# Optimization experiments

Measured on AMD Instinct MI355X. Metric: run time of the kernel, lower is better.

Reference implementation:

```python
import jax, jax.numpy as jnp
import numpy as np

B, N, D = 32, 1024, 768
E_TOK, E_CH, TOP_K = 4, 4, 2
E = E_TOK + E_CH
HN, HD = 4 * N, 4 * D  # hidden dims of token / channel mixers


def setup_inputs() -> dict:
    key = jax.random.key(0)
    ks = jax.random.split(key, 10)
    s = 0.02
    return {
        "x": jax.random.normal(ks[0], (B, N, D), jnp.float32),
        "router_w": jax.random.normal(ks[1], (E, D), jnp.float32) * s,
        # token mixers: fc1 (N->HN), fc2 (HN->N), stacked over E_TOK experts
        "tok_w1": jax.random.normal(ks[2], (E_TOK, HN, N), jnp.float32) * s,
        "tok_b1": jnp.zeros((E_TOK, HN), jnp.float32),
        "tok_w2": jax.random.normal(ks[3], (E_TOK, N, HN), jnp.float32) * s,
        "tok_b2": jnp.zeros((E_TOK, N), jnp.float32),
        # channel mixers: fc1 (D->HD), fc2 (HD->D), stacked over E_CH experts
        "ch_w1": jax.random.normal(ks[4], (E_CH, HD, D), jnp.float32) * s,
        "ch_b1": jnp.zeros((E_CH, HD), jnp.float32),
        "ch_w2": jax.random.normal(ks[5], (E_CH, D, HD), jnp.float32) * s,
        "ch_b2": jnp.zeros((E_CH, D), jnp.float32),
    }


def _gelu(x):
    return jax.nn.gelu(x, approximate=True)  # matches nn.GELU(approximate='tanh')


def reference(x, router_w, tok_w1, tok_b1, tok_w2, tok_b2, ch_w1, ch_b1, ch_w2, ch_b2):
    b = x.shape[0]
    # --- router: mean-pooled tokens -> logits over 8 experts ---
    router_logits = x.mean(axis=1) @ router_w.T                 # (B, E)
    router_probs = jax.nn.softmax(router_logits, axis=-1)
    top_w, top_i = jax.lax.top_k(router_probs, TOP_K)           # (B, k)
    top_w = top_w / top_w.sum(axis=-1, keepdims=True)
    # per-sample dense combine weights: zero for unselected experts
    combine = jnp.zeros((b, E), x.dtype).at[
        jnp.arange(b)[:, None], top_i
    ].add(top_w)                                                # (B, E)

    # --- token mixer experts (mix across N), stacked over experts ---
    xt = x.transpose(0, 2, 1)                                    # (B, D, N)
    h = _gelu(jnp.einsum('bdn,ehn->ebdh', xt, tok_w1) + tok_b1[:, None, None, :])
    tok_out = (jnp.einsum('ebdh,enh->ebdn', h, tok_w2)
               + tok_b2[:, None, None, :]).transpose(0, 1, 3, 2)  # (E_tok, B, N, D)

    # --- channel mixer experts (mix across D) ---
    g = _gelu(jnp.einsum('bnd,ehd->ebnh', x, ch_w1) + ch_b1[:, None, None, :])
    ch_out = jnp.einsum('ebnh,edh->ebnd', g, ch_w2) + ch_b2[:, None, None, :]  # (E_ch, B, N, D)

    all_out = jnp.concatenate([tok_out, ch_out], axis=0)        # (E, B, N, D)
    output = jnp.einsum('ebnd,be->bnd', all_out, combine)

    # --- Switch-style load-balancing aux loss ---
    top1 = top_i[:, 0]
    expert_mask = jax.nn.one_hot(top1, E, dtype=x.dtype)        # (B, E)
    aux_loss = E * jnp.sum(router_probs.mean(axis=0) * expert_mask.mean(axis=0))
    return output, aux_loss
```

## Files before the change

### kernel.cpp

```cpp
#include <hip/hip_runtime.h>
#include <cstdint>
#include <cstddef>

#define Bsz 32
#define Nn 1024
#define Dd 768
#define NE_TOK 4
#define NE 8
#define HN 4096
#define HD 3072
#define INTER_ELEMS (768 * 4096)
#define CHUNK 16

typedef __bf16 bf16x8 __attribute__((ext_vector_type(8)));
typedef float f32x4 __attribute__((ext_vector_type(4)));
typedef unsigned int __attribute__((address_space(1))) as1_uint;
typedef unsigned int __attribute__((address_space(3))) as3_uint;

__device__ __forceinline__ unsigned short f2bf(float f) {
  union { float f; unsigned u; } c; c.f = f;
  unsigned u = c.u;
  u += 0x7fffu + ((u >> 16) & 1u);
  return (unsigned short)(u >> 16);
}

__device__ __forceinline__ float gelu_f(float x) {
  float t = tanhf(0.7978845608028654f * (x + 0.044715f * x * x * x));
  return 0.5f * x * (1.0f + t);
}

__device__ __forceinline__ void async_cp16(const unsigned short* g, unsigned short* l) {
  __builtin_amdgcn_global_load_lds((as1_uint*)(void*)g, (as3_uint*)(void*)l, 16, 0, 0);
}

__device__ __forceinline__ void gemm_core(const unsigned short* Ag, const unsigned short* Bg,
                                          int K, int tm, int tn,
                                          unsigned short* sA, unsigned short* sB,
                                          f32x4 acc[4][4]) {
  const int tid = threadIdx.x;
  const int wave = tid >> 6;
  const int lane = tid & 63;
  const int wr = (wave >> 1) * 64;
  const int wc = (wave & 1) * 64;

  f32x4 zero = {0.f, 0.f, 0.f, 0.f};
#pragma unroll
  for (int i = 0; i < 4; ++i)
#pragma unroll
    for (int j = 0; j < 4; ++j) acc[i][j] = zero;

  const int q0 = wave * 2, q1 = wave * 2 + 1;
  const int c0 = q0 * 64 + lane, c1 = q1 * 64 + lane;
  const int ar0 = c0 >> 2, as0 = (c0 & 3) * 8;
  const int ar1 = c1 >> 2, as1 = (c1 & 3) * 8;
  const unsigned short* Ag0 = Ag + (size_t)(tm * 128 + ar0) * K + as0;
  const unsigned short* Ag1 = Ag + (size_t)(tm * 128 + ar1) * K + as1;
  const unsigned short* Bg0 = Bg + (size_t)(tn * 128 + ar0) * K + as0;
  const unsigned short* Bg1 = Bg + (size_t)(tn * 128 + ar1) * K + as1;
  unsigned short* sA0 = sA + q0 * 512;
  unsigned short* sA1 = sA + q1 * 512;
  unsigned short* sB0 = sB + q0 * 512;
  unsigned short* sB1 = sB + q1 * 512;

  const int fro = (lane & 15) * 32 + (lane >> 4) * 8;

  for (int k0 = 0; k0 < K; k0 += 32) {
    async_cp16(Ag0 + k0, sA0);
    async_cp16(Ag1 + k0, sA1);
    async_cp16(Bg0 + k0, sB0);
    async_cp16(Bg1 + k0, sB1);
    __syncthreads();

    bf16x8 a[4], bb[4];
#pragma unroll
    for (int i = 0; i < 4; ++i)
      a[i] = *(const bf16x8*)(sA + (wr + i * 16) * 32 + fro);
#pragma unroll
    for (int j = 0; j < 4; ++j)
      bb[j] = *(const bf16x8*)(sB + (wc + j * 16) * 32 + fro);
#pragma unroll
    for (int i = 0; i < 4; ++i)
#pragma unroll
      for (int j = 0; j < 4; ++j)
        acc[i][j] = __builtin_amdgcn_mfma_f32_16x16x32_bf16(a[i], bb[j], acc[i][j], 0, 0, 0);
    __syncthreads();
  }
}


__global__ void mean_kernel(const float* __restrict__ x, float* __restrict__ xmean) {
  int idx = blockIdx.x * 256 + threadIdx.x;
  int b = idx / Dd, d = idx - b * Dd;
  const float* p = x + (size_t)b * Nn * Dd + d;
  float s = 0.f;
#pragma unroll 8
  for (int n = 0; n < Nn; ++n) s += p[(size_t)n * Dd];
  xmean[idx] = s * (1.0f / Nn);
}

__global__ void router_kernel(const float* __restrict__ xmean, const float* __restrict__ rw,
                              int* __restrict__ topi, float* __restrict__ topw,
                              float* __restrict__ aux_out) {
  __shared__ float probs[Bsz][NE];
  __shared__ int top1[Bsz];
  int t = threadIdx.x;
  for (int p = t; p < Bsz * NE; p += 64) {
    int b = p >> 3, e = p & 7;
    const float* xm = xmean + b * Dd;
    const float* w = rw + e * Dd;
    float s = 0.f;
    for (int i = 0; i < Dd; ++i) s += xm[i] * w[i];
    probs[b][e] = s;
  }
  __syncthreads();
  if (t < Bsz) {
    float mx = -1e30f;
    for (int e = 0; e < NE; ++e) mx = fmaxf(mx, probs[t][e]);
    float pe[NE]; float sum = 0.f;
    for (int e = 0; e < NE; ++e) { pe[e] = expf(probs[t][e] - mx); sum += pe[e]; }
    float inv = 1.f / sum;
    for (int e = 0; e < NE; ++e) { pe[e] *= inv; probs[t][e] = pe[e]; }
    int i0 = 0;
    for (int e = 1; e < NE; ++e) if (pe[e] > pe[i0]) i0 = e;
    int i1 = (i0 == 0) ? 1 : 0;
    for (int e = 0; e < NE; ++e) if (e != i0 && pe[e] > pe[i1]) i1 = e;
    float ws2 = pe[i0] + pe[i1];
    topi[t * 2] = i0; topi[t * 2 + 1] = i1;
    topw[t * 2] = pe[i0] / ws2; topw[t * 2 + 1] = pe[i1] / ws2;
    top1[t] = i0;
  }
  __syncthreads();
  if (t == 0) {
    float aux = 0.f;
    for (int e = 0; e < NE; ++e) {
      float pm = 0.f; int cnt = 0;
      for (int b = 0; b < Bsz; ++b) { pm += probs[b][e]; if (top1[b] == e) cnt++; }
      aux += (pm / Bsz) * ((float)cnt / Bsz);
    }
    aux_out[0] = aux * NE;
  }
}

__global__ void convert_kernel(const float* __restrict__ src, unsigned short* __restrict__ dst,
                               int n4) {
  int i = blockIdx.x * 256 + threadIdx.x;
  if (i < n4) {
    const float4 v = ((const float4*)src)[i];
    ushort4 o = make_ushort4(f2bf(v.x), f2bf(v.y), f2bf(v.z), f2bf(v.w));
    ((ushort4*)dst)[i] = o;
  }
}

__global__ void transpose_kernel(const float* __restrict__ x,
                                 unsigned short* __restrict__ xbf,
                                 unsigned short* __restrict__ xtbf) {
  __shared__ unsigned short tile[64][66];
  const int b = blockIdx.z;
  const int d0 = blockIdx.x * 64;
  const int n0 = blockIdx.y * 64;
  const int tc = threadIdx.x & 63;
  const int tr = threadIdx.x >> 6;
  const float* xb = x + (size_t)b * Nn * Dd;
#pragma unroll
  for (int i = 0; i < 16; ++i) {
    int row = tr * 16 + i;
    unsigned short v = f2bf(xb[(size_t)(n0 + row) * Dd + d0 + tc]);
    tile[row][tc] = v;
    xbf[(size_t)b * Nn * Dd + (size_t)(n0 + row) * Dd + d0 + tc] = v;
  }
  __syncthreads();
#pragma unroll
  for (int i = 0; i < 16; ++i) {
    int drow = tr * 16 + i;
    xtbf[(size_t)b * Dd * Nn + (size_t)(d0 + drow) * Nn + n0 + tc] = tile[tc][drow];
  }
}

__global__ __launch_bounds__(256, 2) void l1_kernel(
    const unsigned short* __restrict__ xbf, const unsigned short* __restrict__ xtbf,
    const unsigned short* __restrict__ w1t, const unsigned short* __restrict__ w1c,
    const float* __restrict__ b1t, const float* __restrict__ b1c,
    const int* __restrict__ topi, unsigned short* __restrict__ inter, int slot, int b0) {
  __shared__ unsigned short sA[4096];
  __shared__ unsigned short sB[4096];
  const int y = blockIdx.y;
  const int b = b0 + y;
  const int e = topi[b * 2 + slot];
  const int tile = blockIdx.x;
  const unsigned short *A, *Bm;
  const float* bias;
  int K, ldc, tm, tn;
  if (e < NE_TOK) {
    A = xtbf + (size_t)b * Dd * Nn;
    Bm = w1t + (size_t)e * HN * Nn;
    bias = b1t + e * HN;
    K = Nn; ldc = HN;
    tm = tile >> 5; tn = tile & 31;
  } else {
    A = xbf + (size_t)b * Nn * Dd;
    Bm = w1c + (size_t)(e - 4) * HD * Dd;
    bias = b1c + (e - 4) * HD;
    K = Dd; ldc = HD;
    tm = tile / 24; tn = tile - tm * 24;
  }
  unsigned short* C = inter + (size_t)y * INTER_ELEMS;
  f32x4 acc[4][4];
  gemm_core(A, Bm, K, tm, tn, sA, sB, acc);

  const int lane = threadIdx.x & 63, wave = threadIdx.x >> 6;
  const int wr = (wave >> 1) * 64, wc = (wave & 1) * 64;
  const int r0 = tm * 128 + wr + (lane >> 4) * 4;
  const int c0 = tn * 128 + wc + (lane & 15);
#pragma unroll
  for (int i = 0; i < 4; ++i)
#pragma unroll
    for (int j = 0; j < 4; ++j) {
      int col = c0 + j * 16;
      float bcol = bias[col];
#pragma unroll
      for (int r = 0; r < 4; ++r) {
        int row = r0 + i * 16 + r;
        float v = acc[i][j][r] + bcol;
        C[(size_t)row * ldc + col] = f2bf(gelu_f(v));
      }
    }
}

__global__ __launch_bounds__(256, 2) void l2_kernel(
    const unsigned short* __restrict__ inter,
    const unsigned short* __restrict__ w2t, const unsigned short* __restrict__ w2c,
    const float* __restrict__ b2t, const float* __restrict__ b2c,
    const int* __restrict__ topi, const float* __restrict__ topw,
    float* __restrict__ out, int slot, int b0) {
  __shared__ unsigned short sA[4096];
  __shared__ unsigned short sB[4096];
  const int y = blockIdx.y;
  const int b = b0 + y;
  const int e = topi[b * 2 + slot];
  const float wgt = topw[b * 2 + slot];
  const int tile = blockIdx.x;
  const int tm = tile / 6, tn = tile - tm * 6;
  const bool tok = (e < NE_TOK);
  const unsigned short* ib = inter + (size_t)y * INTER_ELEMS;
  const unsigned short *A, *Bm;
  int K;
  if (tok) { A = w2t + (size_t)e * Nn * HN; Bm = ib; K = HN; }
  else     { A = ib; Bm = w2c + (size_t)(e - 4) * Dd * HD; K = HD; }
  f32x4 acc[4][4];
  gemm_core(A, Bm, K, tm, tn, sA, sB, acc);

  float* C = out + (size_t)b * Nn * Dd;
  const int lane = threadIdx.x & 63, wave = threadIdx.x >> 6;
  const int wr = (wave >> 1) * 64, wc = (wave & 1) * 64;
  const int r0 = tm * 128 + wr + (lane >> 4) * 4;
  const int c0 = tn * 128 + wc + (lane & 15);
#pragma unroll
  for (int i = 0; i < 4; ++i)
#pragma unroll
    for (int j = 0; j < 4; ++j) {
      int col = c0 + j * 16;
#pragma unroll
      for (int r = 0; r < 4; ++r) {
        int row = r0 + i * 16 + r;
        float bias = tok ? b2t[e * Nn + row] : b2c[(e - 4) * Dd + col];
        float v = (acc[i][j][r] + bias) * wgt;
        size_t idx = (size_t)row * Dd + col;
        if (slot == 0) C[idx] = v;
        else           C[idx] += v;
      }
    }
}

extern "C" void kernel_launch(void* const* d_in, const int* in_sizes, int n_in,
                              void* d_out, int out_size, void* d_ws, size_t ws_size,
                              hipStream_t stream) {
  const float* x       = (const float*)d_in[0];
  const float* rw      = (const float*)d_in[1];
  const float* tok_w1  = (const float*)d_in[2];
  const float* tok_b1  = (const float*)d_in[3];
  const float* tok_w2  = (const float*)d_in[4];
  const float* tok_b2  = (const float*)d_in[5];
  const float* ch_w1   = (const float*)d_in[6];
  const float* ch_b1   = (const float*)d_in[7];
  const float* ch_w2   = (const float*)d_in[8];
  const float* ch_b2   = (const float*)d_in[9];
  float* out = (float*)d_out;

  char* ws = (char*)d_ws;
  float* xmean = (float*)ws;            ws += (size_t)Bsz * Dd * 4;
  int* topi    = (int*)ws;              ws += 256;
  float* topw  = (float*)ws;            ws += 256;
  unsigned short* xbf  = (unsigned short*)ws; ws += (size_t)Bsz * Nn * Dd * 2;
  unsigned short* xtbf = (unsigned short*)ws; ws += (size_t)Bsz * Nn * Dd * 2;
  unsigned short* w1t  = (unsigned short*)ws; ws += (size_t)NE_TOK * HN * Nn * 2;
  unsigned short* w2t  = (unsigned short*)ws; ws += (size_t)NE_TOK * Nn * HN * 2;
  unsigned short* w1c  = (unsigned short*)ws; ws += (size_t)NE_TOK * HD * Dd * 2;
  unsigned short* w2c  = (unsigned short*)ws; ws += (size_t)NE_TOK * Dd * HD * 2;
  unsigned short* inter = (unsigned short*)ws;

  mean_kernel<<<(Bsz * Dd) / 256, 256, 0, stream>>>(x, xmean);
  router_kernel<<<1, 64, 0, stream>>>(xmean, rw, topi, topw, out + (size_t)Bsz * Nn * Dd);
  convert_kernel<<<16384, 256, 0, stream>>>(tok_w1, w1t, (NE_TOK * HN * Nn) / 4);
  convert_kernel<<<16384, 256, 0, stream>>>(tok_w2, w2t, (NE_TOK * Nn * HN) / 4);
  convert_kernel<<<9216, 256, 0, stream>>>(ch_w1, w1c, (NE_TOK * HD * Dd) / 4);
  convert_kernel<<<9216, 256, 0, stream>>>(ch_w2, w2c, (NE_TOK * Dd * HD) / 4);
  transpose_kernel<<<dim3(12, 16, Bsz), 256, 0, stream>>>(x, xbf, xtbf);

  for (int slot = 0; slot < 2; ++slot)
    for (int c = 0; c < 2; ++c) {
      l1_kernel<<<dim3(192, CHUNK), 256, 0, stream>>>(xbf, xtbf, w1t, w1c, tok_b1, ch_b1,
                                                      topi, inter, slot, c * CHUNK);
      l2_kernel<<<dim3(48, CHUNK), 256, 0, stream>>>(inter, w2t, w2c, tok_b2, ch_b2,
                                                     topi, topw, out, slot, c * CHUNK);
    }
}
```

Measured before the change: 1.761 ms.

## Double-buffer GEMM shared tiles and XOR-swizzle LDS layout

The GEMM core now keeps two shared-memory buffers, so the async copy of the next K tile is issued before the MFMAs on the current tile, and there is one barrier per iteration instead of two. The position of each 16-byte chunk in LDS is XOR-swizzled on both the write side and the fragment-read side to cut bank conflicts. Shared memory per block doubles to 32 KB, which may limit occupancy. Correctness depends on the async copies having completed by the barrier.

```diff
diff --git a/kernel.cpp b/kernel.cpp
--- a/kernel.cpp
+++ b/kernel.cpp
@@ -51,8 +51,8 @@
 
   const int q0 = wave * 2, q1 = wave * 2 + 1;
   const int c0 = q0 * 64 + lane, c1 = q1 * 64 + lane;
-  const int ar0 = c0 >> 2, as0 = (c0 & 3) * 8;
-  const int ar1 = c1 >> 2, as1 = (c1 & 3) * 8;
+  const int ar0 = c0 >> 2, as0 = ((c0 ^ (c0 >> 3)) & 3) * 8;
+  const int ar1 = c1 >> 2, as1 = ((c1 ^ (c1 >> 3)) & 3) * 8;
   const unsigned short* Ag0 = Ag + (size_t)(tm * 128 + ar0) * K + as0;
   const unsigned short* Ag1 = Ag + (size_t)(tm * 128 + ar1) * K + as1;
   const unsigned short* Bg0 = Bg + (size_t)(tn * 128 + ar0) * K + as0;
@@ -62,28 +62,41 @@
   unsigned short* sB0 = sB + q0 * 512;
   unsigned short* sB1 = sB + q1 * 512;
 
-  const int fro = (lane & 15) * 32 + (lane >> 4) * 8;
-
+  const int swz = ((lane >> 4) ^ (lane >> 1)) & 3;
+  const int fro = (lane & 15) * 32 + swz * 8;
+
+  async_cp16(Ag0, sA0);
+  async_cp16(Ag1, sA1);
+  async_cp16(Bg0, sB0);
+  async_cp16(Bg1, sB1);
+  __syncthreads();
+
+  int cur = 0;
   for (int k0 = 0; k0 < K; k0 += 32) {
-    async_cp16(Ag0 + k0, sA0);
-    async_cp16(Ag1 + k0, sA1);
-    async_cp16(Bg0 + k0, sB0);
-    async_cp16(Bg1 + k0, sB1);
-    __syncthreads();
-
+    const int k1 = k0 + 32;
+    if (k1 < K) {
+      const int nb = (cur ^ 1) * 4096;
+      async_cp16(Ag0 + k1, sA0 + nb);
+      async_cp16(Ag1 + k1, sA1 + nb);
+      async_cp16(Bg0 + k1, sB0 + nb);
+      async_cp16(Bg1 + k1, sB1 + nb);
+    }
+    const unsigned short* pA = sA + cur * 4096;
+    const unsigned short* pB = sB + cur * 4096;
     bf16x8 a[4], bb[4];
 #pragma unroll
     for (int i = 0; i < 4; ++i)
-      a[i] = *(const bf16x8*)(sA + (wr + i * 16) * 32 + fro);
+      a[i] = *(const bf16x8*)(pA + (wr + i * 16) * 32 + fro);
 #pragma unroll
     for (int j = 0; j < 4; ++j)
-      bb[j] = *(const bf16x8*)(sB + (wc + j * 16) * 32 + fro);
+      bb[j] = *(const bf16x8*)(pB + (wc + j * 16) * 32 + fro);
 #pragma unroll
     for (int i = 0; i < 4; ++i)
 #pragma unroll
       for (int j = 0; j < 4; ++j)
         acc[i][j] = __builtin_amdgcn_mfma_f32_16x16x32_bf16(a[i], bb[j], acc[i][j], 0, 0, 0);
     __syncthreads();
+    cur ^= 1;
   }
 }
 
@@ -181,8 +194,8 @@
     const unsigned short* __restrict__ w1t, const unsigned short* __restrict__ w1c,
     const float* __restrict__ b1t, const float* __restrict__ b1c,
     const int* __restrict__ topi, unsigned short* __restrict__ inter, int slot, int b0) {
-  __shared__ unsigned short sA[4096];
-  __shared__ unsigned short sB[4096];
+  __shared__ unsigned short sA[8192];
+  __shared__ unsigned short sB[8192];
   const int y = blockIdx.y;
   const int b = b0 + y;
   const int e = topi[b * 2 + slot];
@@ -232,8 +245,8 @@
     const float* __restrict__ b2t, const float* __restrict__ b2c,
     const int* __restrict__ topi, const float* __restrict__ topw,
     float* __restrict__ out, int slot, int b0) {
-  __shared__ unsigned short sA[4096];
-  __shared__ unsigned short sB[4096];
+  __shared__ unsigned short sA[8192];
+  __shared__ unsigned short sB[8192];
   const int y = blockIdx.y;
   const int b = b0 + y;
   const int e = topi[b * 2 + slot];
```

Measured after the change: 1.757 ms. Within noise of the previous version (-0.2%).
